# Kernel optimization log

Measured on AMD Instinct MI355X. Metric: run time of the kernel, lower is better.

## Reference

```python
import jax, jax.numpy as jnp
import numpy as np

B, T, D_EMB, D_H = 4, 4096, 512, 64


def setup_inputs() -> dict:
    key = jax.random.key(0)
    ks = jax.random.split(key, 7)
    s_in = 1.0 / np.sqrt(D_EMB)
    return {
        "x": jax.random.normal(ks[0], (B, T, D_EMB), jnp.float32),
        "Wq_w": jax.random.normal(ks[1], (D_H, D_EMB), jnp.float32) * s_in,
        "Wq_b": jax.random.normal(ks[2], (D_H,), jnp.float32) * 0.02,
        "Wk_w": jax.random.normal(ks[3], (D_H, D_EMB), jnp.float32) * s_in,
        "Wk_b": jax.random.normal(ks[4], (D_H,), jnp.float32) * 0.02,
        "Wv_w": jax.random.normal(ks[5], (D_H, D_EMB), jnp.float32) * s_in,
        "Wv_b": jax.random.normal(ks[6], (D_H,), jnp.float32) * 0.02,
    }


def reference(x, Wq_w, Wq_b, Wk_w, Wk_b, Wv_w, Wv_b):
    # Q,K,V: [B,T,d_h] via torch.nn.Linear semantics (x @ W.T + b)
    Q = jnp.einsum("btc,hc->bth", x, Wq_w) + Wq_b
    K = jnp.einsum("btc,hc->bth", x, Wk_w) + Wk_b
    V = jnp.einsum("btc,hc->bth", x, Wv_w) + Wv_b
    # raw scores [B,T,T], causal mask, softmax, then post-softmax scale by sqrt(d_h)
    scores = jnp.einsum("bqh,bkh->bqk", Q, K)
    causal = jnp.tril(jnp.ones((T, T), dtype=bool))
    scores = jnp.where(causal, scores, -jnp.inf)
    alpha = jax.nn.softmax(scores, axis=-1) * jnp.sqrt(jnp.float32(D_H))
    return jnp.einsum("bqk,bkh->bqh", alpha, V)
```

## Files before the change

kernel.cpp:

```cpp
#include <hip/hip_runtime.h>
#include <hip/hip_fp16.h>
#include <math.h>

#define B 4
#define T 4096
#define DEMB 512
#define DH 64
#define NSPLIT 8
#define NPTILE 16
#define LOG2E 1.44269504088896340736f

typedef _Float16 f16;
typedef __attribute__((ext_vector_type(4))) _Float16 f16x4;
typedef __attribute__((ext_vector_type(8))) _Float16 f16x8;
typedef __attribute__((ext_vector_type(4))) float f32x4;

__device__ __forceinline__ float fexp2(float x) {
    return __builtin_amdgcn_exp2f(x);
}

__global__ __launch_bounds__(256) void convert_w(
    const float* __restrict__ Wq, const float* __restrict__ Wk,
    const float* __restrict__ Wv, f16* __restrict__ Wf)
{
    const int idx = blockIdx.x * 256 + threadIdx.x;
    const int row = idx >> 9;
    const int k   = idx & 511;
    const float* W = row < 64 ? Wq : (row < 128 ? Wk : Wv);
    Wf[idx] = (f16)W[(row & 63) * DEMB + k];
}

__global__ __launch_bounds__(512) void proj_mfma(
    const float* __restrict__ x, const f16* __restrict__ Wfg,
    const float* __restrict__ bq, const float* __restrict__ bk,
    const float* __restrict__ bv,
    f16* __restrict__ Qf, f16* __restrict__ Kf, f16* __restrict__ Vt)
{
    __shared__ f16 xs[32][136];
    __shared__ f16 Ws[192][136];

    const int tid  = threadIdx.x;
    const int wv   = tid >> 6;
    const int lane = tid & 63;
    const int i16  = lane & 15;
    const int quad = lane >> 4;
    const int rg   = wv >> 2;
    const int nh   = wv & 3;
    const size_t r0 = (size_t)blockIdx.x * 32;

    const int xrow = tid >> 4, xg = tid & 15;
    float4 xa, xb;
    f16x8 wpre[6];

    {
        xa = *(const float4*)(x + (r0 + xrow) * DEMB + xg * 8);
        xb = *(const float4*)(x + (r0 + xrow) * DEMB + xg * 8 + 4);
#pragma unroll
        for (int u = 0; u < 6; ++u) {
            const int idx = tid + 512 * u;
            const int row = idx >> 4, g = idx & 15;
            wpre[u] = *(const f16x8*)(Wfg + (size_t)row * DEMB + g * 8);
        }
    }

    f32x4 acc[3];
    const f32x4 zero = {0.f, 0.f, 0.f, 0.f};
#pragma unroll
    for (int n = 0; n < 3; ++n) acc[n] = zero;

    for (int cc = 0; cc < DEMB; cc += 128) {
        __syncthreads();
        {
            f16x8 h = {(f16)xa.x, (f16)xa.y, (f16)xa.z, (f16)xa.w,
                       (f16)xb.x, (f16)xb.y, (f16)xb.z, (f16)xb.w};
            *(f16x8*)&xs[xrow][xg * 8] = h;
        }
#pragma unroll
        for (int u = 0; u < 6; ++u) {
            const int idx = tid + 512 * u;
            const int row = idx >> 4, g = idx & 15;
            *(f16x8*)&Ws[row][g * 8] = wpre[u];
        }
        __syncthreads();

        if (cc + 128 < DEMB) {
            const int cn = cc + 128;
            xa = *(const float4*)(x + (r0 + xrow) * DEMB + cn + xg * 8);
            xb = *(const float4*)(x + (r0 + xrow) * DEMB + cn + xg * 8 + 4);
#pragma unroll
            for (int u = 0; u < 6; ++u) {
                const int idx = tid + 512 * u;
                const int row = idx >> 4, g = idx & 15;
                wpre[u] = *(const f16x8*)(Wfg + (size_t)row * DEMB + cn + g * 8);
            }
        }

#pragma unroll
        for (int kk = 0; kk < 4; ++kk) {
            const f16x8 af = *(const f16x8*)&xs[rg * 16 + i16][kk * 32 + quad * 8];
#pragma unroll
            for (int n = 0; n < 3; ++n) {
                const f16x8 bf = *(const f16x8*)&Ws[(nh * 3 + n) * 16 + i16][kk * 32 + quad * 8];
                acc[n] = __builtin_amdgcn_mfma_f32_16x16x32_f16(af, bf, acc[n], 0, 0, 0);
            }
        }
    }

    const size_t bb = r0 / T;
    const size_t t0 = r0 - bb * T;
#pragma unroll
    for (int n = 0; n < 3; ++n) {
        const int col = (nh * 3 + n) * 16 + i16;
        const int m = col >> 6, h = col & 63;
        const float bias = (m == 0 ? bq : (m == 1 ? bk : bv))[h];
#pragma unroll
        for (int r = 0; r < 4; ++r) {
            const int row = rg * 16 + quad * 4 + r;
            const float v = acc[n][r] + bias;
            const size_t grow = r0 + row;
            if (m == 0)      Qf[grow * DH + h] = (f16)(v * LOG2E);
            else if (m == 1) Kf[grow * DH + h] = (f16)v;
            else             Vt[(bb * DH + h) * T + t0 + row] = (f16)v;
        }
    }
}

__global__ __launch_bounds__(512) void attn_partial(
    const f16* __restrict__ Qf, const f16* __restrict__ Kf,
    const f16* __restrict__ Vt,
    f16* __restrict__ Opart, float* __restrict__ mpart,
    float* __restrict__ lpart)
{
    __shared__ f16 Ks[2][64][72], Vs[2][64][72];
    __shared__ f16 Pl[8][16][72];

    const int tid  = threadIdx.x;
    const int wv   = tid >> 6;
    const int lane = tid & 63;
    const int i16  = lane & 15;
    const int quad = lane >> 4;

    const int s    = blockIdx.x & 7;
    const int p    = 15 - ((blockIdx.x >> 3) & 15);
    const int bb   = blockIdx.x >> 7;
    const size_t base = (size_t)bb * T;
    const int row0 = p * 256;
    const int cmax = 4 * p + 3;
    if (s > cmax) return;
    const int rowg0 = row0 + wv * 16;
    const int rowg1 = row0 + (wv + 8) * 16;

    f16x8 qf00, qf01, qf10, qf11;
    {
        const f16* q0 = Qf + (base + rowg0 + i16) * DH;
        const f16* q1 = Qf + (base + rowg1 + i16) * DH;
        qf00 = *(const f16x8*)(q0 + quad * 8);
        qf01 = *(const f16x8*)(q0 + 32 + quad * 8);
        qf10 = *(const f16x8*)(q1 + quad * 8);
        qf11 = *(const f16x8*)(q1 + 32 + quad * 8);
    }

    f32x4 oacc[2][4];
    float mm[2] = {-INFINITY, -INFINITY}, ll[2] = {0.f, 0.f};
    const f32x4 zero = {0.f, 0.f, 0.f, 0.f};
#pragma unroll
    for (int j = 0; j < 2; ++j)
#pragma unroll
        for (int n = 0; n < 4; ++n) oacc[j][n] = zero;

    const int srow = tid >> 3, sg = tid & 7;
    f16x8 kpre, vpre;
    {
        const int kb = s << 6;
        kpre = *(const f16x8*)(Kf + (base + kb + srow) * DH + sg * 8);
        vpre = *(const f16x8*)(Vt + ((size_t)bb * DH + srow) * T + kb + sg * 8);
    }

    int buf = 0;
    for (int c = s; c <= cmax; c += NSPLIT) {
        *(f16x8*)&Ks[buf][srow][sg * 8] = kpre;
        *(f16x8*)&Vs[buf][srow][sg * 8] = vpre;
        __syncthreads();

        const int cn = c + NSPLIT;
        if (cn <= cmax) {
            const int kbn = cn << 6;
            kpre = *(const f16x8*)(Kf + (base + kbn + srow) * DH + sg * 8);
            vpre = *(const f16x8*)(Vt + ((size_t)bb * DH + srow) * T + kbn + sg * 8);
        }

        const int kb = c << 6;
        const bool a0 = kb <= rowg0, a1 = kb <= rowg1;
        if (a1) {
            f32x4 st[2][4];
#pragma unroll
            for (int kt = 0; kt < 4; ++kt) {
                const f16x8 kf0 = *(const f16x8*)&Ks[buf][kt * 16 + i16][quad * 8];
                const f16x8 kf1 = *(const f16x8*)&Ks[buf][kt * 16 + i16][32 + quad * 8];
                if (a0) {
                    f32x4 a = __builtin_amdgcn_mfma_f32_16x16x32_f16(kf0, qf00, zero, 0, 0, 0);
                    st[0][kt] = __builtin_amdgcn_mfma_f32_16x16x32_f16(kf1, qf01, a, 0, 0, 0);
                }
                {
                    f32x4 a = __builtin_amdgcn_mfma_f32_16x16x32_f16(kf0, qf10, zero, 0, 0, 0);
                    st[1][kt] = __builtin_amdgcn_mfma_f32_16x16x32_f16(kf1, qf11, a, 0, 0, 0);
                }
            }
            f16x8 pf[2][2];
#pragma unroll
            for (int j = 0; j < 2; ++j) {
                if (j == 0 && !a0) continue;
                const int rowg = j == 0 ? rowg0 : rowg1;
                if (kb + 63 > rowg) {
#pragma unroll
                    for (int kt = 0; kt < 4; ++kt)
#pragma unroll
                        for (int r = 0; r < 4; ++r)
                            if (kb + kt * 16 + quad * 4 + r > rowg + i16)
                                st[j][kt][r] = -INFINITY;
                }
                float mx = -INFINITY;
#pragma unroll
                for (int kt = 0; kt < 4; ++kt)
#pragma unroll
                    for (int r = 0; r < 4; ++r) mx = fmaxf(mx, st[j][kt][r]);
                mx = fmaxf(mx, __shfl_xor(mx, 16, 64));
                mx = fmaxf(mx, __shfl_xor(mx, 32, 64));
                const float mnew = fmaxf(mm[j], mx);
                const float alpha = fexp2(mm[j] - mnew);
                mm[j] = mnew;
                float sum = 0.f;
#pragma unroll
                for (int kt = 0; kt < 4; ++kt) {
                    f16x4 pk;
#pragma unroll
                    for (int r = 0; r < 4; ++r) {
                        const f16 pb = (f16)fexp2(st[j][kt][r] - mnew);
                        pk[r] = pb;
                        sum += (float)pb;
                    }
                    *(f16x4*)&Pl[wv][i16][kt * 16 + quad * 4] = pk;
                }
                sum += __shfl_xor(sum, 16, 64);
                sum += __shfl_xor(sum, 32, 64);
                ll[j] = ll[j] * alpha + sum;
#pragma unroll
                for (int n = 0; n < 4; ++n) oacc[j][n] *= alpha;
                pf[j][0] = *(const f16x8*)&Pl[wv][i16][quad * 8];
                pf[j][1] = *(const f16x8*)&Pl[wv][i16][32 + quad * 8];
            }
#pragma unroll
            for (int mt = 0; mt < 4; ++mt) {
                const f16x8 vf0 = *(const f16x8*)&Vs[buf][mt * 16 + i16][quad * 8];
                const f16x8 vf1 = *(const f16x8*)&Vs[buf][mt * 16 + i16][32 + quad * 8];
                if (a0) {
                    oacc[0][mt] = __builtin_amdgcn_mfma_f32_16x16x32_f16(vf0, pf[0][0], oacc[0][mt], 0, 0, 0);
                    oacc[0][mt] = __builtin_amdgcn_mfma_f32_16x16x32_f16(vf1, pf[0][1], oacc[0][mt], 0, 0, 0);
                }
                oacc[1][mt] = __builtin_amdgcn_mfma_f32_16x16x32_f16(vf0, pf[1][0], oacc[1][mt], 0, 0, 0);
                oacc[1][mt] = __builtin_amdgcn_mfma_f32_16x16x32_f16(vf1, pf[1][1], oacc[1][mt], 0, 0, 0);
            }
        }
        buf ^= 1;
    }

    f16* Ob = Opart + (size_t)blockIdx.x * (256 * 64);
#pragma unroll
    for (int j = 0; j < 2; ++j) {
        const int prow = (wv + 8 * j) * 16 + i16;
#pragma unroll
        for (int mt = 0; mt < 4; ++mt) {
            f16x4 pk = {(f16)oacc[j][mt][0], (f16)oacc[j][mt][1],
                        (f16)oacc[j][mt][2], (f16)oacc[j][mt][3]};
            *(f16x4*)&Ob[prow * 64 + mt * 16 + quad * 4] = pk;
        }
        if (quad == 0) {
            mpart[(size_t)blockIdx.x * 256 + prow] = mm[j];
            lpart[(size_t)blockIdx.x * 256 + prow] = ll[j];
        }
    }
}

__global__ __launch_bounds__(256) void attn_combine(
    const f16* __restrict__ Opart, const float* __restrict__ mpart,
    const float* __restrict__ lpart, float* __restrict__ O)
{
    __shared__ float ws[16][NSPLIT];
    __shared__ float scl[16];

    const int tid = threadIdx.x;
    const int sub = blockIdx.x & 15;
    const int p   = (blockIdx.x >> 4) & 15;
    const int bb  = blockIdx.x >> 8;
    const size_t pb0 = (size_t)bb * 128 + (15 - p) * NSPLIT;
    const int nact = min(NSPLIT, 4 * p + 4);
    const int r0c  = sub * 16;

    if (tid < 16) {
        const int row = r0c + tid;
        float m[NSPLIT];
        float M = -INFINITY;
        for (int q = 0; q < nact; ++q) {
            m[q] = mpart[(pb0 + q) * 256 + row];
            M = fmaxf(M, m[q]);
        }
        float L = 0.f;
        for (int q = 0; q < nact; ++q) {
            const float w = fexp2(m[q] - M);
            ws[tid][q] = w;
            L += w * lpart[(pb0 + q) * 256 + row];
        }
        scl[tid] = 8.0f / L;
    }
    __syncthreads();

    const int rowl = tid >> 4;
    const int c4   = tid & 15;
    const int row  = r0c + rowl;
    float a0 = 0.f, a1 = 0.f, a2 = 0.f, a3 = 0.f;
    for (int q = 0; q < nact; ++q) {
        const f16x4 v = *(const f16x4*)&Opart[(pb0 + q) * (256 * 64) + row * 64 + c4 * 4];
        const float w = ws[rowl][q];
        a0 += w * (float)v[0]; a1 += w * (float)v[1];
        a2 += w * (float)v[2]; a3 += w * (float)v[3];
    }
    const float s = scl[rowl];
    const float4 o = {a0 * s, a1 * s, a2 * s, a3 * s};
    *(float4*)&O[((size_t)bb * T + p * 256 + row) * DH + c4 * 4] = o;
}

extern "C" void kernel_launch(void* const* d_in, const int* in_sizes, int n_in,
                              void* d_out, int out_size, void* d_ws, size_t ws_size,
                              hipStream_t stream) {
    const float* x  = (const float*)d_in[0];
    const float* Wq = (const float*)d_in[1];
    const float* bq = (const float*)d_in[2];
    const float* Wk = (const float*)d_in[3];
    const float* bk = (const float*)d_in[4];
    const float* Wv = (const float*)d_in[5];
    const float* bv = (const float*)d_in[6];

    const size_t N  = (size_t)B * T * DH;
    f16* Qf = (f16*)d_ws;
    f16* Kf = Qf + N;
    f16* Vt = Kf + N;
    f16* Wf = Vt + N;
    f16* Opart = Wf + (size_t)192 * DEMB;
    float* mpart = (float*)(Opart + (size_t)512 * 256 * 64);
    float* lpart = mpart + (size_t)512 * 256;

    convert_w<<<dim3(192 * DEMB / 256), dim3(256), 0, stream>>>(Wq, Wk, Wv, Wf);
    proj_mfma<<<dim3(B * T / 32), dim3(512), 0, stream>>>(
        x, Wf, bq, bk, bv, Qf, Kf, Vt);
    attn_partial<<<dim3(B * NPTILE * NSPLIT), dim3(512), 0, stream>>>(
        Qf, Kf, Vt, Opart, mpart, lpart);
    attn_combine<<<dim3(B * NPTILE * 16), dim3(256), 0, stream>>>(
        Opart, mpart, lpart, (float*)d_out);
}
```

Baseline: 132.6 us.

## Fuse split-K combine into attention kernel via last-block ticket counter

Removes the separate attn_combine launch. Each attention block bumps an atomic ticket for its (batch, query-tile) after writing its partial results, and the last block to arrive does the merge. Tickets are reset in convert_w. This saves a kernel launch and its tail, but the final block per tile now runs a serial combine over 256 rows, which may lengthen the critical path. It also adds fences and an atomic to every block.

Result: slower. 328.0 us (+147.3%).

```diff
diff --git a/kernel.cpp b/kernel.cpp
--- a/kernel.cpp
+++ b/kernel.cpp
@@ -21,8 +21,10 @@
 
 __global__ __launch_bounds__(256) void convert_w(
     const float* __restrict__ Wq, const float* __restrict__ Wk,
-    const float* __restrict__ Wv, f16* __restrict__ Wf)
+    const float* __restrict__ Wv, f16* __restrict__ Wf,
+    int* __restrict__ tickets)
 {
+    if (blockIdx.x == 0 && threadIdx.x < B * NPTILE) tickets[threadIdx.x] = 0;
     const int idx = blockIdx.x * 256 + threadIdx.x;
     const int row = idx >> 9;
     const int k   = idx & 511;
@@ -129,10 +131,12 @@
     const f16* __restrict__ Qf, const f16* __restrict__ Kf,
     const f16* __restrict__ Vt,
     f16* __restrict__ Opart, float* __restrict__ mpart,
-    float* __restrict__ lpart)
+    float* __restrict__ lpart, int* __restrict__ tickets,
+    float* __restrict__ O)
 {
     __shared__ f16 Ks[2][64][72], Vs[2][64][72];
     __shared__ f16 Pl[8][16][72];
+    __shared__ int is_last_s;
 
     const int tid  = threadIdx.x;
     const int wv   = tid >> 6;
@@ -141,11 +145,13 @@
     const int quad = lane >> 4;
 
     const int s    = blockIdx.x & 7;
-    const int p    = 15 - ((blockIdx.x >> 3) & 15);
+    const int pidx = (blockIdx.x >> 3) & 15;
+    const int p    = 15 - pidx;
     const int bb   = blockIdx.x >> 7;
     const size_t base = (size_t)bb * T;
     const int row0 = p * 256;
     const int cmax = 4 * p + 3;
+    const int nact = min(NSPLIT, cmax + 1);
     if (s > cmax) return;
     const int rowg0 = row0 + wv * 16;
     const int rowg1 = row0 + (wv + 8) * 16;
@@ -279,25 +285,22 @@
             lpart[(size_t)blockIdx.x * 256 + prow] = ll[j];
         }
     }
-}
-
-__global__ __launch_bounds__(256) void attn_combine(
-    const f16* __restrict__ Opart, const float* __restrict__ mpart,
-    const float* __restrict__ lpart, float* __restrict__ O)
-{
-    __shared__ float ws[16][NSPLIT];
-    __shared__ float scl[16];
-
-    const int tid = threadIdx.x;
-    const int sub = blockIdx.x & 15;
-    const int p   = (blockIdx.x >> 4) & 15;
-    const int bb  = blockIdx.x >> 8;
-    const size_t pb0 = (size_t)bb * 128 + (15 - p) * NSPLIT;
-    const int nact = min(NSPLIT, 4 * p + 4);
-    const int r0c  = sub * 16;
-
-    if (tid < 16) {
-        const int row = r0c + tid;
+
+    __threadfence();
+    __syncthreads();
+    if (tid == 0) {
+        const int t = atomicAdd(&tickets[bb * NPTILE + pidx], 1);
+        is_last_s = (t == nact - 1);
+    }
+    __syncthreads();
+    if (!is_last_s) return;
+    __threadfence();
+
+    float (*cws)[NSPLIT] = (float (*)[NSPLIT]) & Ks[0][0][0];
+    float* cscl = (float*)&Vs[0][0][0];
+
+    const size_t pb0 = (size_t)bb * 128 + (size_t)pidx * 8;
+    for (int row = tid; row < 256; row += 512) {
         float m[NSPLIT];
         float M = -INFINITY;
         for (int q = 0; q < nact; ++q) {
@@ -307,26 +310,28 @@
         float L = 0.f;
         for (int q = 0; q < nact; ++q) {
             const float w = fexp2(m[q] - M);
-            ws[tid][q] = w;
+            cws[row][q] = w;
             L += w * lpart[(pb0 + q) * 256 + row];
         }
-        scl[tid] = 8.0f / L;
+        cscl[row] = 8.0f / L;
     }
     __syncthreads();
 
-    const int rowl = tid >> 4;
-    const int c4   = tid & 15;
-    const int row  = r0c + rowl;
-    float a0 = 0.f, a1 = 0.f, a2 = 0.f, a3 = 0.f;
-    for (int q = 0; q < nact; ++q) {
-        const f16x4 v = *(const f16x4*)&Opart[(pb0 + q) * (256 * 64) + row * 64 + c4 * 4];
-        const float w = ws[rowl][q];
-        a0 += w * (float)v[0]; a1 += w * (float)v[1];
-        a2 += w * (float)v[2]; a3 += w * (float)v[3];
-    }
-    const float s = scl[rowl];
-    const float4 o = {a0 * s, a1 * s, a2 * s, a3 * s};
-    *(float4*)&O[((size_t)bb * T + p * 256 + row) * DH + c4 * 4] = o;
+    const int c4 = tid & 15;
+#pragma unroll
+    for (int it = 0; it < 8; ++it) {
+        const int row = (tid >> 4) + 32 * it;
+        float a0 = 0.f, a1 = 0.f, a2 = 0.f, a3 = 0.f;
+        for (int q = 0; q < nact; ++q) {
+            const f16x4 v = *(const f16x4*)&Opart[(pb0 + q) * (256 * 64) + row * 64 + c4 * 4];
+            const float w = cws[row][q];
+            a0 += w * (float)v[0]; a1 += w * (float)v[1];
+            a2 += w * (float)v[2]; a3 += w * (float)v[3];
+        }
+        const float sc = cscl[row];
+        const float4 o = {a0 * sc, a1 * sc, a2 * sc, a3 * sc};
+        *(float4*)&O[((size_t)bb * T + row0 + row) * DH + c4 * 4] = o;
+    }
 }
 
 extern "C" void kernel_launch(void* const* d_in, const int* in_sizes, int n_in,
@@ -348,12 +353,12 @@
     f16* Opart = Wf + (size_t)192 * DEMB;
     float* mpart = (float*)(Opart + (size_t)512 * 256 * 64);
     float* lpart = mpart + (size_t)512 * 256;
-
-    convert_w<<<dim3(192 * DEMB / 256), dim3(256), 0, stream>>>(Wq, Wk, Wv, Wf);
+    int*   tickets = (int*)(lpart + (size_t)512 * 256);
+
+    convert_w<<<dim3(192 * DEMB / 256), dim3(256), 0, stream>>>(
+        Wq, Wk, Wv, Wf, tickets);
     proj_mfma<<<dim3(B * T / 32), dim3(512), 0, stream>>>(
         x, Wf, bq, bk, bv, Qf, Kf, Vt);
     attn_partial<<<dim3(B * NPTILE * NSPLIT), dim3(512), 0, stream>>>(
-        Qf, Kf, Vt, Opart, mpart, lpart);
-    attn_combine<<<dim3(B * NPTILE * 16), dim3(256), 0, stream>>>(
-        Opart, mpart, lpart, (float*)d_out);
-}
+        Qf, Kf, Vt, Opart, mpart, lpart, tickets, (float*)d_out);
+}
```
